# Kernel tuning notes

Measured on AMD Instinct MI355X. Metric: run time of the kernel, lower is better.

The kernel has to match this reference:

```python
import jax, jax.numpy as jnp
import numpy as np

B, T, E, D, V, L, A = 32, 800, 512, 1024, 5000, 149, 512
SOS, EOS = 1, 2


def setup_inputs() -> dict:
    key = jax.random.key(0)
    ks = jax.random.split(key, 20)
    s = 0.02
    inp = {
        'hpad': jax.random.normal(ks[0], (B, T, E), dtype=jnp.float32),
        'hlen': jax.random.randint(ks[1], (B,), T // 2, T + 1),
        'ys': jax.random.randint(ks[2], (B, L), 3, V),
        # embedding + output projection
        'embed': jax.random.normal(ks[3], (V, D), dtype=jnp.float32) * s,
        'W_out': jax.random.normal(ks[4], (V, D), dtype=jnp.float32) * s,
        'b_out': jnp.zeros((V,), dtype=jnp.float32),
        # additive attention params
        'W_enc': jax.random.normal(ks[5], (E, A), dtype=jnp.float32) * s,
        'W_dec': jax.random.normal(ks[6], (D, A), dtype=jnp.float32) * s,
        'v_att': jax.random.normal(ks[7], (A,), dtype=jnp.float32) * s,
        # LSTMCell layer 0: input = [ey; att_c] of size D+E
        'W_ih0': jax.random.normal(ks[8], (4 * D, D + E), dtype=jnp.float32) * s,
        'b_ih0': jnp.zeros((4 * D,), dtype=jnp.float32),
        'W_hh0': jax.random.normal(ks[9], (4 * D, D), dtype=jnp.float32) * s,
        'b_hh0': jnp.zeros((4 * D,), dtype=jnp.float32),
        # LSTMCell layer 1: input = z0 of size D
        'W_ih1': jax.random.normal(ks[10], (4 * D, D), dtype=jnp.float32) * s,
        'b_ih1': jnp.zeros((4 * D,), dtype=jnp.float32),
        'W_hh1': jax.random.normal(ks[11], (4 * D, D), dtype=jnp.float32) * s,
        'b_hh1': jnp.zeros((4 * D,), dtype=jnp.float32),
    }
    return inp


def _lstm_cell(x, h, c, W_ih, b_ih, W_hh, b_hh):
    # torch.nn.LSTMCell gate order: i, f, g, o
    g = x @ W_ih.T + b_ih + h @ W_hh.T + b_hh
    i, f, gg, o = jnp.split(g, 4, axis=-1)
    c2 = jax.nn.sigmoid(f) * c + jax.nn.sigmoid(i) * jnp.tanh(gg)
    h2 = jax.nn.sigmoid(o) * jnp.tanh(c2)
    return h2, c2


def reference(hpad, hlen, ys, embed, W_out, b_out, W_enc, W_dec, v_att,
              W_ih0, b_ih0, W_hh0, b_hh0, W_ih1, b_ih1, W_hh1, b_hh1):
    mask = jnp.arange(T)[None, :] < hlen[:, None]          # [B,T]
    hpad = hpad * mask[..., None]                          # mask_by_length
    ys_in = jnp.concatenate([jnp.full((B, 1), SOS, ys.dtype), ys], axis=1)   # [B,L+1]
    ys_out = jnp.concatenate([ys, jnp.full((B, 1), EOS, ys.dtype)], axis=1)  # [B,L+1]
    eys = embed[ys_in]                                     # [B,L+1,D]
    pe = jnp.einsum('bte,ea->bta', hpad, W_enc)            # precomputed enc proj

    def step(carry, ey):
        z0, c0, z1, c1 = carry
        # additive attention: e = v^T tanh(W_enc h + W_dec z0)
        e = jnp.einsum('bta,a->bt', jnp.tanh(pe + (z0 @ W_dec)[:, None, :]), v_att)
        e = jnp.where(mask, e, -1e30)
        w = jax.nn.softmax(e, axis=-1)                     # [B,T]
        att_c = jnp.einsum('bt,bte->be', w, hpad)          # [B,E]
        z0, c0 = _lstm_cell(jnp.concatenate([ey, att_c], axis=1), z0, c0,
                            W_ih0, b_ih0, W_hh0, b_hh0)
        z1, c1 = _lstm_cell(z0, z1, c1, W_ih1, b_ih1, W_hh1, b_hh1)
        logits = z1 @ W_out.T + b_out                      # [B,V]
        return (z0, c0, z1, c1), logits

    z = jnp.zeros((B, D), dtype=hpad.dtype)
    carry0 = (z, z, z, z)
    _, logits = jax.lax.scan(step, carry0, eys.transpose(1, 0, 2))  # [L+1,B,V]
    logits = logits.transpose(1, 0, 2)                     # [B,L+1,V]

    logp = jax.nn.log_softmax(logits, axis=-1)
    nll = -jnp.take_along_axis(logp, ys_out[..., None], axis=-1)[..., 0]
    # F.cross_entropy mean, then * (mean(len ys_in) - 1) = * L
    loss = nll.mean() * L
    acc = (jnp.argmax(logits, axis=-1) == ys_out).mean()
    return loss, acc
```

## Files before the change

kernel.cpp:

```cpp
#include <hip/hip_runtime.h>


typedef unsigned short u16;
typedef unsigned char u8;
typedef unsigned int u32;
typedef long long i64;
typedef unsigned long long u64;
typedef float f32x4 __attribute__((ext_vector_type(4)));
typedef float f32x2 __attribute__((ext_vector_type(2)));
typedef short s16x8 __attribute__((ext_vector_type(8)));

constexpr int cB = 32, cT = 800, cE = 512, cD = 1024, cV = 5000, cL = 149,
              cNS = 150, cA = 512;
constexpr int SOS = 1, EOS = 2;
constexpr int NBLK = 256;
constexpr float DS = 1.0f / 128.0f;

constexpr int AFLAG = 0;
constexpr int Z0FLAG = 256;
constexpr int Z1FLAG = 384;
constexpr int SFLAG = 512;
constexpr int ZDONE = 768;

__device__ __forceinline__ float bf2f(u16 x){
  union { u32 u; float f; } v; v.u = ((u32)x) << 16; return v.f;
}
__device__ __forceinline__ u16 f2bf(float f){
  union { float f; u32 u; } v; v.f = f;
  u32 r = v.u + 0x7FFFu + ((v.u >> 16) & 1u);
  return (u16)(r >> 16);
}
__device__ __forceinline__ float frcp(float x){ return __builtin_amdgcn_rcpf(x); }
__device__ __forceinline__ float fsigm(float x){ return frcp(1.f + __expf(-x)); }
__device__ __forceinline__ float ftanh(float x){
  float u = __expf(2.f * x);
  return 1.f - 2.f * frcp(u + 1.f);
}
__device__ __forceinline__ f32x4 MFMA(s16x8 a, s16x8 b, f32x4 c){
  return __builtin_amdgcn_mfma_f32_16x16x32_bf16(a, b, c, 0, 0, 0);
}
__device__ __forceinline__ f32x4 MFMA8(i64 a, i64 b, f32x4 c){
  return __builtin_amdgcn_mfma_f32_16x16x32_fp8_fp8(a, b, c, 0, 0, 0);
}
__device__ __forceinline__ s16x8 LD8(const u16* p){ return *(const s16x8*)p; }
__device__ __forceinline__ u8 f2fp8(float x){
// ... 36 lines not shown
}
__device__ __forceinline__ void atomic_pk_bf16(u32* dst, u32 data){
  asm volatile("global_atomic_pk_add_bf16 %0, %1, off"
               :: "v"(dst), "v"(data) : "memory");
}

__device__ __forceinline__ void pollge(const u32* f, int n, u32 target){
  const int lane = threadIdx.x & 63;
  for(;;){
    bool ok = true;
    for (int i = lane; i < n; i += 64) ok &= (ld_su(f + i) >= target);
    if (__all(ok)) break;
    __builtin_amdgcn_s_sleep(1);
  }
}
__device__ __forceinline__ void sig(u32* f, u32 v){
  asm volatile("s_waitcnt vmcnt(0)" ::: "memory");
  st_su(f, v);
}

__global__ void k_init(u32* ctl, u32* qt, float* c0, float* c1, u8* z1f8,
                       u32* att_pk, float* att_l, u32* hh1t){
  int i = blockIdx.x * blockDim.x + threadIdx.x, n = gridDim.x * blockDim.x;
  for (int k = i; k < 1024; k += n) ctl[k] = 0;
  for (int k = i; k < cB * cA; k += n) qt[k] = 0;
  for (int k = i; k < 2 * cB * cD; k += n){ c0[k] = 0.f; c1[k] = 0.f; }
  for (int k = i; k < cB * cD / 4; k += n) ((u32*)z1f8)[k] = 0;
  for (int k = i; k < 2 * cB * 256; k += n) att_pk[k] = 0;
  for (int k = i; k < 2 * cB; k += n) att_l[k] = 0.f;
  for (int k = i; k < cB * 4096; k += n) hh1t[k] = 0xFFFF0000u;
}

__global__ void k_cvt(const float* __restrict__ s, u16* __restrict__ d, int n4){
  int i = blockIdx.x * blockDim.x + threadIdx.x, st = gridDim.x * blockDim.x;
  for (int k = i; k < n4; k += st){
    float4 v = ((const float4*)s)[k];
    ushort4 o; o.x = f2bf(v.x); o.y = f2bf(v.y); o.z = f2bf(v.z); o.w = f2bf(v.w);
    ((ushort4*)d)[k] = o;
  }
}

__global__ void k_cvt8I(const float* __restrict__ s, u8* __restrict__ d, int n){
  int i = blockIdx.x * blockDim.x + threadIdx.x, st = gridDim.x * blockDim.x;
  for (int k = i; k < n; k += st){
    int row = k >> 6, grp = k & 63;
    const float4* p = (const float4*)(s + (size_t)row * 512 + grp * 8);
    float4 v0 = p[0], v1 = p[1];
// ... 9 lines not shown
  int cmask = (1 << cshift) - 1;
  for (int k = i; k < n; k += st){
    int r = k >> cshift, c = k & cmask;
    d[k] = f2bf(s[(size_t)r * srcld + coff + c]);
  }
}

__global__ void k_transp(const float* __restrict__ s, u16* __restrict__ d, int n,
                         int rshift, int csrc){
  int i = blockIdx.x * blockDim.x + threadIdx.x, st = gridDim.x * blockDim.x;
  int mask = (1 << rshift) - 1;
  for (int k = i; k < n; k += st){
    int dd = k & mask, a = k >> rshift;
    d[k] = f2bf(s[(size_t)dd * csrc + a]);
  }
}

__global__ void k_bias(const float* a, const float* b, float* o, int n){
  int i = blockIdx.x * blockDim.x + threadIdx.x, st = gridDim.x * blockDim.x;
  for (int k = i; k < n; k += st) o[k] = a[k] + b[k];
}

__global__ void k_wf8perm(const float* __restrict__ s, u8* __restrict__ d,
                          int n4, int kshift, int srcld, int coff){
  int i = blockIdx.x * blockDim.x + threadIdx.x, st = gridDim.x * blockDim.x;
  int kmask = (1 << kshift) - 1;
  for (int k = i; k < n4; k += st){
    int flat = k * 4;
    int R = flat >> kshift, kk = flat & kmask;
    int j = R >> 5, jj = R & 31, g = jj >> 3, c = jj & 7;
    const float* p = s + (size_t)(g * 1024 + j * 8 + c) * srcld + coff + kk;
    ((u32*)d)[k] = pk4(p[0]*16.f, p[1]*16.f, p[2]*16.f, p[3]*16.f);
  }
}

__global__ void k_wf8(const float* __restrict__ s, u8* __restrict__ d, int n4){
  int i = blockIdx.x * blockDim.x + threadIdx.x, st = gridDim.x * blockDim.x;
  for (int k = i; k < n4; k += st){
    float4 v = ((const float4*)s)[k];
    ((u32*)d)[k] = pk4(v.x*16.f, v.y*16.f, v.z*16.f, v.w*16.f);
  }
}

__global__ void k_wf8t(const float* __restrict__ s, u8* __restrict__ d, int n4){
  int i = blockIdx.x * blockDim.x + threadIdx.x, st = gridDim.x * blockDim.x;
  for (int k = i; k < n4; k += st){
    int flat = k * 4;
    int a = flat >> 10, dd = flat & 1023;
    ((u32*)d)[k] = pk4(s[(size_t)(dd+0)*512 + a]*16.f,
                       s[(size_t)(dd+1)*512 + a]*16.f,
                       s[(size_t)(dd+2)*512 + a]*16.f,
                       s[(size_t)(dd+3)*512 + a]*16.f);
  }
}
// ... 73 lines not shown
  int hi4 = (l >> 4) * 4;
  #pragma unroll
  for (int i = 0; i < 4; ++i)
    #pragma unroll
    for (int j = 0; j < 8; ++j){
      int jc = n0 + j * 16 + col;
      float bj = bih0[jc] + bhh0[jc];
      #pragma unroll
      for (int r = 0; r < 4; ++r){
        int row = m0 + i * 16 + hi4 + r;
        if (row < 4800){
          float val = acc[i][j][r] + bj;
          eyproj[(size_t)row * 4096 + jc] = f2bf(val);
          if (row < 32) g0t[(size_t)row * 4096 + jc] = (u32)f2bf(val);
        }
      }
    }
}

struct LoopArgs {
  const int* hlen;
  const u8* ph8;
  const u16* eyproj;
  const u8* Wapf8; const u8* Whh1f8; const u8* Wih1f8; const u8* Whh0f8;
  const u8* WdecTf8;
  const float* vatt; const float* bias01;
  u32* qt; u32* att_pk; float* att_l;
  u32* g0t; u32* hh1t; u8* z0f8; u8* z1f8;
  float* c0; float* c1; u16* z1all;
  u32* ctl;
};

constexpr int SPZ = 1048;
constexpr int SPA = 536;

struct P1Lds { float red[8][512]; float ls[8]; float qsh[512]; };
struct GvLds { u8 x[32 * SPZ]; float acc[8][2][16][17]; };
union LoopLds { P1Lds p1; GvLds gv; };

__device__ __forceinline__ void stage_att(LoopLds& L, const u32* att_pk,
                                          const float* att_l, int tid){
  int r = tid >> 4, cp = (tid & 15) * 16;
  float sc = 8.0f * frcp(ld_sc(att_l + r));
  const u32* src = att_pk + (size_t)r * 256 + cp;
  u64 v[8];
  #pragma unroll
  for (int i = 0; i < 8; ++i) v[i] = ld_sc8(src + i * 2);
// ... 25 lines not shown
template<int KH, int ITERS, int SP>
__device__ __forceinline__ void gemv_reg(const i64* wreg, LoopLds& L, int tid){
  const int w = tid >> 6, l = tid & 63;
  const int col = l & 15, kin = 8 * (l >> 4);
  const int kh = (KH == 4) ? (w & 3) : (w & 1);
  constexpr int KB = ITERS * 32;
  const u8* xr = &L.gv.x[col * SP + kh * KB + kin];
  f32x4 a0 = {0.f,0.f,0.f,0.f}, a1 = {0.f,0.f,0.f,0.f};
  #pragma unroll
  for (int kc = 0; kc < ITERS; ++kc){
    i64 x0 = *(const i64*)(xr + kc * 32);
    i64 x1 = *(const i64*)(xr + 16 * SP + kc * 32);
    a0 = MFMA8(x0, wreg[kc], a0);
    a1 = MFMA8(x1, wreg[kc], a1);
  }
  const int hi4 = (l >> 4) * 4;
  #pragma unroll
  for (int r = 0; r < 4; ++r){
    L.gv.acc[w][0][hi4 + r][col] = a0[r];
    L.gv.acc[w][1][hi4 + r][col] = a1[r];
  }
}

__global__ __launch_bounds__(512, 1) void k_loop(LoopArgs g_){
  __shared__ __align__(16) LoopLds L;
  __shared__ __align__(16) u8 ph8_lds[100 * 1024];
  const int blk = blockIdx.x, tid = threadIdx.x;
  const int w = tid >> 6, l = tid & 63;
  const int col = l & 15, kin = 8 * (l >> 4);
  const int b_att = blk >> 3, oct = blk & 7;
  const int hl = g_.hlen[b_att];
  const int t0 = oct * 100;
  const int t1 = (t0 + 100 < hl) ? t0 + 100 : hl;
  const int nrow = t1 - t0;
  u32* ctl = g_.ctl;
  float vv[8];
  #pragma unroll
  for (int i = 0; i < 8; ++i) vv[i] = g_.vatt[l * 8 + i];
  for (int idx = tid; idx < nrow * 64; idx += 512){
    int rr = idx >> 6, gg = idx & 63;
    *(uint4*)&ph8_lds[rr * 1024 + gg * 16] =
        *(const uint4*)(g_.ph8 + ((size_t)b_att * cT + t0 + rr) * 1024 + gg * 16);
  }
  i64 wB[8], wC[16];
  {
    const int nt4 = w >> 2, kh4 = w & 3;
    const int nt2 = w >> 1, kh2 = w & 1;
    if (blk < 128){
      const u8* wr = g_.Wapf8 + (size_t)blk * 32 * 512 +
                     (size_t)(nt4 * 16 + col) * 512 + kh4 * 128 + kin;
      #pragma unroll
      for (int kc = 0; kc < 4; ++kc) wB[kc] = *(const i64*)(wr + kc * 32);
      const u8* wr2 = g_.Wih1f8 + (size_t)blk * 32 * 1024 +
                      (size_t)(nt4 * 16 + col) * 1024 + kh4 * 256 + kin;
      #pragma unroll
      for (int kc = 0; kc < 8; ++kc) wC[kc] = *(const i64*)(wr2 + kc * 32);
    } else {
      const u8* wr = g_.Whh1f8 + (size_t)(blk - 128) * 32 * 1024 +
                     (size_t)(nt4 * 16 + col) * 1024 + kh4 * 256 + kin;
      #pragma unroll
      for (int kc = 0; kc < 8; ++kc) wB[kc] = *(const i64*)(wr + kc * 32);
      if (blk < 192){
        const u8* wr2 = g_.Whh0f8 + (size_t)(blk - 128) * 64 * 1024 +
                        (size_t)(nt2 * 16 + col) * 1024 + kh2 * 512 + kin;
        #pragma unroll
        for (int kc = 0; kc < 16; ++kc) wC[kc] = *(const i64*)(wr2 + kc * 32);
      } else if (blk < 208){
        const u8* wr2 = g_.WdecTf8 + (size_t)(blk - 192) * 32 * 1024 +
                        (size_t)(nt4 * 16 + col) * 1024 + kh4 * 256 + kin;
        #pragma unroll
        for (int kc = 0; kc < 8; ++kc) wC[kc] = *(const i64*)(wr2 + kc * 32);
      }
    }
  }
  __syncthreads();

  for (int s = 0; s < cNS; ++s){
    const int p = s & 1;
    if (nrow > 0){
      if (w == 0){
        const u32* qrow = g_.qt + b_att * cA + l * 8;
        const u64 tmask = 0xFFFF0000FFFF0000ULL;
        const u64 texp = ((u64)(u32)s << 48) | ((u64)(u32)s << 16);
        u64 qw[4];
        for(;;){
          bool ok = true;
          #pragma unroll
          for (int i = 0; i < 4; ++i){
            qw[i] = ld_sc8(qrow + i * 2);
            ok &= ((qw[i] & tmask) == texp);
          }
          if (l == 0)
            ok &= (ld_su(&ctl[ZDONE + p * 16]) >= (u32)(s >> 1));
          if (__all(ok)) break;
          __builtin_amdgcn_s_sleep(1);
        }
        #pragma unroll
        for (int i = 0; i < 4; ++i){
          L.p1.qsh[l * 8 + 2*i]     = bf2f((u16)(qw[i] & 0xFFFF));
          L.p1.qsh[l * 8 + 2*i + 1] = bf2f((u16)((qw[i] >> 32) & 0xFFFF));
        }
      }
      __syncthreads();
      float qv[8];
      #pragma unroll
      for (int i = 0; i < 8; ++i) qv[i] = L.p1.qsh[l * 8 + i];
      float acc8[8] = {0.f,0.f,0.f,0.f,0.f,0.f,0.f,0.f};
      float lsum = 0.f;
      for (int t = t0 + w; t < t1; t += 8){
        uint4 v = *(const uint4*)&ph8_lds[(t - t0) * 1024 + l * 16];
        float x[8]; unpack8(v.x, v.y, x);
        float e_ = 0.f;
        #pragma unroll
        for (int i = 0; i < 8; ++i) e_ += vv[i] * ftanh(x[i] + qv[i]);
        #pragma unroll
        for (int m = 1; m < 64; m <<= 1) e_ += __shfl_xor(e_, m, 64);
        float wt = __expf(e_);
        lsum += wt;
        float h[8]; unpack8(v.z, v.w, h);
        #pragma unroll
        for (int i = 0; i < 8; ++i) acc8[i] = fmaf(wt, h[i], acc8[i]);
      }
      *(f32x4*)&L.p1.red[w][l * 8]     = *(f32x4*)&acc8[0];
      *(f32x4*)&L.p1.red[w][l * 8 + 4] = *(f32x4*)&acc8[4];
      if (l == 0) L.p1.ls[w] = lsum;
      __syncthreads();
      if (tid < 256){
        float v0 = 0.f, v1 = 0.f;
        #pragma unroll
        for (int ww = 0; ww < 8; ++ww){
          v0 += L.p1.red[ww][tid * 2];
          v1 += L.p1.red[ww][tid * 2 + 1];
        }
        u32 pk = ((u32)f2bf(v1) << 16) | (u32)f2bf(v0);
        atomic_pk_bf16(g_.att_pk + ((size_t)p * cB + b_att) * 256 + tid, pk);
      }
      if (tid == 0){
        float ls = 0.f;
        #pragma unroll
        for (int i = 0; i < 8; ++i) ls += L.p1.ls[i];
        atomicAdd(&g_.att_l[p * cB + b_att], ls);
      }
    }
    __syncthreads();
    if (tid == 0) sig(&ctl[AFLAG + blk], (u32)(s + 1));
    if (blk < 128){
      if (tid < 64) pollge(ctl + AFLAG, 256, (u32)(s + 1));
      __syncthreads();
      stage_att(L, g_.att_pk + (size_t)p * cB * 256, g_.att_l + p * cB, tid);
      __syncthreads();
      if (tid == 0) sig(&ctl[SFLAG + p * 128 + blk], (u32)(s >> 1) + 1u);
      u32 gw[4]; bool gok = true; float cpre = 0.f;
      int bb = tid >> 3, dc = tid & 7, d = blk * 8 + dc;
      if (tid < 256){
        #pragma unroll
        for (int g = 0; g < 4; ++g){
          gw[g] = ld_su(&g_.g0t[(size_t)bb * 4096 + g * 1024 + d]);
          gok &= ((gw[g] >> 16) == (u32)s);
        }
        cpre = g_.c0[(size_t)p * cB * cD + bb * cD + d];
      }
      gemv_reg<4, 4, SPA>(wB, L, tid);
      __syncthreads();
      if (tid < 256){
        while (!__all(gok)){
          gok = true;
          #pragma unroll
          for (int g = 0; g < 4; ++g){
            gw[g] = ld_su(&g_.g0t[(size_t)bb * 4096 + g * 1024 + d]);
            gok &= ((gw[g] >> 16) == (u32)s);
          }
          if (!__all(gok)) __builtin_amdgcn_s_sleep(1);
        }
        int mt = bb >> 4, rr = bb & 15;
        float gate[4];
        #pragma unroll
        for (int g = 0; g < 4; ++g){
          int jj = g * 8 + dc;
          float v = 0.f;
          #pragma unroll
          for (int kh = 0; kh < 4; ++kh)
            v += L.gv.acc[(jj >> 4) * 4 + kh][mt][rr][jj & 15];
          gate[g] = v * DS + bf2f((u16)(gw[g] & 0xFFFF));
        }
        float c = fsigm(gate[1]) * cpre + fsigm(gate[0]) * ftanh(gate[2]);
        float z = fsigm(gate[3]) * ftanh(c);
        g_.c0[(size_t)(p ^ 1) * cB * cD + bb * cD + d] = c;
        st_scb(&g_.z0f8[bb * cD + d], f2fp8(z * 8.f));
      }
      __syncthreads();
      if (tid == 0) sig(&ctl[Z0FLAG + blk], (u32)(s + 1));
    } else {
      if (tid < 64) pollge(ctl + Z1FLAG, 128, (u32)s);
      __syncthreads();
      stage_z(L, g_.z1f8, tid);
      __syncthreads();
      gemv_reg<4, 8, SPZ>(wB, L, tid);
      __syncthreads();
      {
        const int jb = (blk - 128) * 32;
        int bb = tid >> 4, j2 = (tid & 15) * 2;
        int mt = bb >> 4, rr = bb & 15;
        u32 ow[2];
        #pragma unroll
        for (int k = 0; k < 2; ++k){
          int jj = j2 + k;
          float v = 0.f;
          #pragma unroll
          for (int kh = 0; kh < 4; ++kh)
            v += L.gv.acc[(jj >> 4) * 4 + kh][mt][rr][jj & 15];
          ow[k] = ((u32)(s + 1) << 16) | (u32)f2bf(v * DS + g_.bias01[jb + jj]);
        }
        st_sc8(&g_.hh1t[(size_t)bb * 4096 + jb + j2], ((u64)ow[1] << 32) | ow[0]);
      }
    }
    if (blk < 128){
      if (tid < 64) pollge(ctl + Z0FLAG, 128, (u32)(s + 1));
      __syncthreads();
      stage_z(L, g_.z0f8, tid);
      __syncthreads();
      u32 hw[4]; bool hok = true; float cpre = 0.f;
      int bb = tid >> 3, dc = tid & 7, d = blk * 8 + dc;
      if (tid < 256){
        #pragma unroll
        for (int g = 0; g < 4; ++g){
          hw[g] = ld_su(&g_.hh1t[(size_t)bb * 4096 + g * 1024 + d]);
          hok &= ((hw[g] >> 16) == (u32)(s + 1));
        }
        cpre = g_.c1[(size_t)p * cB * cD + bb * cD + d];
      }
      gemv_reg<4, 8, SPZ>(wC, L, tid);
      __syncthreads();
      if (tid < 256){
        while (!__all(hok)){
          hok = true;
          #pragma unroll
          for (int g = 0; g < 4; ++g){
            hw[g] = ld_su(&g_.hh1t[(size_t)bb * 4096 + g * 1024 + d]);
            hok &= ((hw[g] >> 16) == (u32)(s + 1));
          }
          if (!__all(hok)) __builtin_amdgcn_s_sleep(1);
        }
        int mt = bb >> 4, rr = bb & 15;
        float gate[4];
        #pragma unroll
        for (int g = 0; g < 4; ++g){
          int jj = g * 8 + dc;
          float v = 0.f;
          #pragma unroll
          for (int kh = 0; kh < 4; ++kh)
            v += L.gv.acc[(jj >> 4) * 4 + kh][mt][rr][jj & 15];
          gate[g] = v * DS + bf2f((u16)(hw[g] & 0xFFFF));
        }
        float c = fsigm(gate[1]) * cpre + fsigm(gate[0]) * ftanh(gate[2]);
        float z = fsigm(gate[3]) * ftanh(c);
        g_.c1[(size_t)(p ^ 1) * cB * cD + bb * cD + d] = c;
        g_.z1all[((size_t)s + 1) * cB * cD + bb * cD + d] = f2bf(z);
        st_scb(&g_.z1f8[bb * cD + d], f2fp8(z * 8.f));
      }
      __syncthreads();
      if (tid == 0) sig(&ctl[Z1FLAG + blk], (u32)(s + 1));
    } else if (blk < 192){
      if (tid < 64) pollge(ctl + Z0FLAG, 128, (u32)(s + 1));
      __syncthreads();
      stage_z(L, g_.z0f8, tid);
      __syncthreads();
      gemv_reg<2, 16, SPZ>(wC, L, tid);
      __syncthreads();
      if (s < cNS - 1){
        const int jb = (blk - 128) * 64;
        int bb = tid >> 4, j4 = (tid & 15) * 4;
        int mt = bb >> 4, rr = bb & 15;
        const u16* eyr = g_.eyproj + (((size_t)(s + 1) * cB + bb) * 4096) + jb + j4;
        u32 ow[4];
        #pragma unroll
        for (int k = 0; k < 4; ++k){
          int jj = j4 + k;
          float v = 0.f;
          #pragma unroll
          for (int kh = 0; kh < 2; ++kh)
            v += L.gv.acc[(jj >> 4) * 2 + kh][mt][rr][jj & 15];
          ow[k] = ((u32)(s + 1) << 16) | (u32)f2bf(v * DS + bf2f(eyr[k]));
        }
        st_sc8(&g_.g0t[(size_t)bb * 4096 + jb + j4],     ((u64)ow[1] << 32) | ow[0]);
        st_sc8(&g_.g0t[(size_t)bb * 4096 + jb + j4 + 2], ((u64)ow[3] << 32) | ow[2]);
      }
    } else if (blk < 208){
      if (tid < 64) pollge(ctl + Z0FLAG, 128, (u32)(s + 1));
      __syncthreads();
      stage_z(L, g_.z0f8, tid);
      __syncthreads();
      gemv_reg<4, 8, SPZ>(wC, L, tid);
      __syncthreads();
      if (s < cNS - 1){
        const int jb = (blk - 192) * 32;
        int bb = tid >> 4, j2 = (tid & 15) * 2;
        int mt = bb >> 4, rr = bb & 15;
        u32 ow[2];
        #pragma unroll
        for (int k = 0; k < 2; ++k){
          int jj = j2 + k;
          float v = 0.f;
          #pragma unroll
          for (int kh = 0; kh < 4; ++kh)
            v += L.gv.acc[(jj >> 4) * 4 + kh][mt][rr][jj & 15];
          ow[k] = ((u32)(s + 1) << 16) | (u32)f2bf(v * DS);
        }
        st_sc8(&g_.qt[(size_t)bb * cA + jb + j2], ((u64)ow[1] << 32) | ow[0]);
      }
    } else if (blk == 208){
      if (tid < 64) pollge(ctl + SFLAG + p * 128, 128, (u32)(s >> 1) + 1u);
      __syncthreads();
      {
        u32* aa = g_.att_pk + (size_t)p * cB * 256;
        for (int i = tid; i < cB * 256; i += 512) st_su(&aa[i], 0);
        if (tid < cB) st_sc(&g_.att_l[p * cB + tid], 0.f);
      }
      __syncthreads();
      if (tid == 0) sig(&ctl[ZDONE + p * 16], (u32)(s >> 1) + 1u);
    }
  }
}

__global__ __launch_bounds__(256) void k_ce1(const u16* __restrict__ z1all,
    const u16* __restrict__ Woutb, const float* __restrict__ bout,
    const int* __restrict__ ys, float* __restrict__ pmax, float* __restrict__ psum,
    int* __restrict__ pai, float* __restrict__ tgtl){
  int blk = blockIdx.x;
  int sc = blk / 40, vc = blk % 40;
  int tid = threadIdx.x, w = tid >> 6, l = tid & 63;
  int kin = 8 * (l >> 4), col = l & 15;
  int v0 = vc * 128 + w * 32;
  int vA = v0 + col, vB = v0 + 16 + col;
  float boA = (vA < cV) ? bout[vA] : 0.f;
// ... 118 lines not shown
  const int*   hlen = (const int*)d_in[1];
  const int*   ys   = (const int*)d_in[2];
  const float* embed= (const float*)d_in[3];
  const float* Wout = (const float*)d_in[4];
  const float* bout = (const float*)d_in[5];
  const float* Wenc = (const float*)d_in[6];
  const float* Wdec = (const float*)d_in[7];
  const float* vatt = (const float*)d_in[8];
  const float* Wih0 = (const float*)d_in[9];
  const float* bih0 = (const float*)d_in[10];
  const float* Whh0 = (const float*)d_in[11];
  const float* bhh0 = (const float*)d_in[12];
  const float* Wih1 = (const float*)d_in[13];
  const float* bih1 = (const float*)d_in[14];
  const float* Whh1 = (const float*)d_in[15];
  const float* bhh1 = (const float*)d_in[16];
  (void)in_sizes; (void)n_in; (void)out_size; (void)ws_size;

  char* base = (char*)d_ws;
  size_t off = 0;
  auto alloc = [&](size_t bytes) -> void* {
    void* r = base + off; off += (bytes + 255) & ~(size_t)255; return r;
  };
  u32*   ctl     = (u32*)  alloc(1024 * 4);
  u16*   hpadM   = (u16*)  alloc((size_t)cB * cT * cE * 2);
  u8*    ph8     = (u8*)   alloc((size_t)cB * cT * 1024);
  u16*   embb    = (u16*)  alloc((size_t)cV * cD * 2);
  u16*   ey      = (u16*)  alloc((size_t)cNS * cB * cD * 2);
  u16*   eyproj  = (u16*)  alloc((size_t)cNS * cB * 4096 * 2);
  u16*   z1all   = (u16*)  alloc((size_t)(cNS + 1) * cB * cD * 2);
  u16*   WencT   = (u16*)  alloc((size_t)cA * cE * 2);
  u16*   Wih0m   = (u16*)  alloc((size_t)4096 * cD * 2);
  u16*   Woutb   = (u16*)  alloc((size_t)cV * cD * 2);
  u8*    Wapf8   = (u8*)   alloc((size_t)4096 * 512);
  u8*    Wih1f8  = (u8*)   alloc((size_t)4096 * 1024);
  u8*    Whh1f8  = (u8*)   alloc((size_t)4096 * 1024);
  u8*    Whh0f8  = (u8*)   alloc((size_t)4096 * 1024);
  u8*    WdecTf8 = (u8*)   alloc((size_t)512 * 1024);
  float* bias01  = (float*)alloc(4096 * 4);
  u32*   qt      = (u32*)  alloc((size_t)cB * cA * 4);
  u32*   att_pk  = (u32*)  alloc((size_t)2 * cB * 256 * 4);
  float* att_l   = (float*)alloc((size_t)2 * cB * 4);
  u32*   g0t     = (u32*)  alloc((size_t)cB * 4096 * 4);
  u32*   hh1t    = (u32*)  alloc((size_t)cB * 4096 * 4);
  u8*    z0f8    = (u8*)   alloc((size_t)cB * cD);
  u8*    z1f8    = (u8*)   alloc((size_t)cB * cD);
  float* c0      = (float*)alloc((size_t)2 * cB * cD * 4);
  float* c1      = (float*)alloc((size_t)2 * cB * cD * 4);
  float* pmax    = (float*)alloc((size_t)cNS * cB * 40 * 4);
  float* psum    = (float*)alloc((size_t)cNS * cB * 40 * 4);
  int*   pai     = (int*)  alloc((size_t)cNS * cB * 40 * 4);
  float* tgtl    = (float*)alloc((size_t)cNS * cB * 4);
  float* cestep  = (float*)alloc((size_t)cNS * 2 * 4);

  k_init<<<64, 256, 0, stream>>>(ctl, qt, c0, c1, z1f8, att_pk, att_l, hh1t);
  k_cvt<<<2048, 256, 0, stream>>>(hpad, hpadM, cB * cT * cE / 4);
  k_cvt8I<<<1024, 256, 0, stream>>>(hpad, ph8, cB * cT * 64);
  k_cvt<<<2048, 256, 0, stream>>>(embed, embb, cV * cD / 4);
  k_cvt<<<2048, 256, 0, stream>>>(Wout, Woutb, cV * cD / 4);
  k_slice<<<1024, 256, 0, stream>>>(Wih0, Wih0m, 4096 * cD, 10, 1536, 0);
  k_transp<<<256, 256, 0, stream>>>(Wenc, WencT, cA * cE, 9, cA);
  k_bias<<<16, 256, 0, stream>>>(bih1, bhh1, bias01, 4096);
  k_wf8perm<<<512, 256, 0, stream>>>(Wih0, Wapf8, 4096 * 512 / 4, 9, 1536, 1024);
  k_wf8perm<<<1024, 256, 0, stream>>>(Wih1, Wih1f8, 4096 * 1024 / 4, 10, 1024, 0);
  k_wf8<<<1024, 256, 0, stream>>>(Whh1, Whh1f8, 4096 * 1024 / 4);
  k_wf8<<<1024, 256, 0, stream>>>(Whh0, Whh0f8, 4096 * 1024 / 4);
  k_wf8t<<<128, 256, 0, stream>>>(Wdec, WdecTf8, 512 * 1024 / 4);
  k_gather<<<1200, 256, 0, stream>>>(embb, ys, ey, cNS * cB * 128);
  k_pe2<<<200, 512, 0, stream>>>(hpadM, WencT, ph8);
  k_ey2<<<dim3(38, 8), 512, 0, stream>>>(ey, Wih0m, bih0, bhh0, eyproj, g0t);

  LoopArgs la;
  la.hlen = hlen; la.ph8 = ph8; la.eyproj = eyproj;
  la.Wapf8 = Wapf8; la.Whh1f8 = Whh1f8; la.Wih1f8 = Wih1f8;
  la.Whh0f8 = Whh0f8; la.WdecTf8 = WdecTf8;
  la.vatt = vatt; la.bias01 = bias01;
  la.qt = qt; la.att_pk = att_pk; la.att_l = att_l;
  la.g0t = g0t; la.hh1t = hh1t; la.z0f8 = z0f8; la.z1f8 = z1f8;
  la.c0 = c0; la.c1 = c1; la.z1all = z1all; la.ctl = ctl;
  k_loop<<<NBLK, 512, 0, stream>>>(la);

  k_ce1<<<1200, 256, 0, stream>>>(z1all, Woutb, bout, ys, pmax, psum, pai, tgtl);
  k_ce2<<<cNS, 64, 0, stream>>>(pmax, psum, pai, tgtl, ys, cestep);
  k_ce3<<<1, 256, 0, stream>>>(cestep, (float*)d_out);
}
```

Before: 4.028 ms.

## Split persistent loop into 512 blocks with dedicated attention blocks

Doubles the persistent decoder grid to 512 blocks. 256 blocks now do only the attention scoring and read the encoder projection straight from global memory instead of staging it in LDS. The other 256 blocks handle the LSTM layer-0 gate GEMV with 16 columns each, plus the Wdec, Wih1, Whh0 and Whh1 GEMVs, and z0 is double-buffered. The aim is to spread the per-step recurrent work over more CUs and free LDS so more blocks fit per CU. The cost is more flag polling across twice as many blocks, and attention now reads global/L2 memory every step.

```diff
diff --git a/kernel.cpp b/kernel.cpp
--- a/kernel.cpp
+++ b/kernel.cpp
@@ -13,14 +13,13 @@
 constexpr int cB = 32, cT = 800, cE = 512, cD = 1024, cV = 5000, cL = 149,
               cNS = 150, cA = 512;
 constexpr int SOS = 1, EOS = 2;
-constexpr int NBLK = 256;
 constexpr float DS = 1.0f / 128.0f;
 
 constexpr int AFLAG = 0;
 constexpr int Z0FLAG = 256;
-constexpr int Z1FLAG = 384;
-constexpr int SFLAG = 512;
-constexpr int ZDONE = 768;
+constexpr int Z1FLAG = 512;
+constexpr int SFLAG = 768;
+constexpr int ZDONE = 1536;
 
 __device__ __forceinline__ float bf2f(u16 x){
   union { u32 u; float f; } v; v.u = ((u32)x) << 16; return v.f;
@@ -103,7 +102,7 @@
 __global__ void k_init(u32* ctl, u32* qt, float* c0, float* c1, u8* z1f8,
                        u32* att_pk, float* att_l, u32* hh1t){
   int i = blockIdx.x * blockDim.x + threadIdx.x, n = gridDim.x * blockDim.x;
-  for (int k = i; k < 1024; k += n) ctl[k] = 0;
+  for (int k = i; k < 2048; k += n) ctl[k] = 0;
   for (int k = i; k < cB * cA; k += n) qt[k] = 0;
   for (int k = i; k < 2 * cB * cD; k += n){ c0[k] = 0.f; c1[k] = 0.f; }
   for (int k = i; k < cB * cD / 4; k += n) ((u32*)z1f8)[k] = 0;
@@ -159,14 +158,14 @@
 }
 
 __global__ void k_wf8perm(const float* __restrict__ s, u8* __restrict__ d,
-                          int n4, int kshift, int srcld, int coff){
+                          int n4, int kshift, int srcld, int coff, int gshift){
   int i = blockIdx.x * blockDim.x + threadIdx.x, st = gridDim.x * blockDim.x;
-  int kmask = (1 << kshift) - 1;
+  int kmask = (1 << kshift) - 1, gmask = (1 << gshift) - 1;
   for (int k = i; k < n4; k += st){
     int flat = k * 4;
     int R = flat >> kshift, kk = flat & kmask;
-    int j = R >> 5, jj = R & 31, g = jj >> 3, c = jj & 7;
-    const float* p = s + (size_t)(g * 1024 + j * 8 + c) * srcld + coff + kk;
+    int c = R & gmask, g = (R >> gshift) & 3, j = R >> (gshift + 2);
+    const float* p = s + (size_t)(g * 1024 + (j << gshift) + c) * srcld + coff + kk;
     ((u32*)d)[k] = pk4(p[0]*16.f, p[1]*16.f, p[2]*16.f, p[3]*16.f);
   }
 }
@@ -286,7 +285,7 @@
   const int* hlen;
   const u8* ph8;
   const u16* eyproj;
-  const u8* Wapf8; const u8* Whh1f8; const u8* Wih1f8; const u8* Whh0f8;
+  const u8* Wap16; const u8* Whh1f8; const u8* Wih1f8; const u8* Whh0f8;
   const u8* WdecTf8;
   const float* vatt; const float* bias01;
   u32* qt; u32* att_pk; float* att_l;
@@ -358,183 +357,160 @@
   }
 }
 
-__global__ __launch_bounds__(512, 1) void k_loop(LoopArgs g_){
+__device__ __forceinline__ void gemv16(const i64* wreg, LoopLds& L, int tid){
+  const int w = tid >> 6, l = tid & 63;
+  const int col = l & 15, kin = 8 * (l >> 4);
+  const u8* xr = &L.gv.x[col * SPA + w * 64 + kin];
+  f32x4 a0 = {0.f,0.f,0.f,0.f}, a1 = {0.f,0.f,0.f,0.f};
+  #pragma unroll
+  for (int kc = 0; kc < 2; ++kc){
+    i64 x0 = *(const i64*)(xr + kc * 32);
+    i64 x1 = *(const i64*)(xr + 16 * SPA + kc * 32);
+    a0 = MFMA8(x0, wreg[kc], a0);
+    a1 = MFMA8(x1, wreg[kc], a1);
+  }
+  const int hi4 = (l >> 4) * 4;
+  #pragma unroll
+  for (int r = 0; r < 4; ++r){
+    L.gv.acc[w][0][hi4 + r][col] = a0[r];
+    L.gv.acc[w][1][hi4 + r][col] = a1[r];
+  }
+}
+
+__global__ __launch_bounds__(512, 4) void k_loop(LoopArgs g_){
   __shared__ __align__(16) LoopLds L;
-  __shared__ __align__(16) u8 ph8_lds[100 * 1024];
   const int blk = blockIdx.x, tid = threadIdx.x;
   const int w = tid >> 6, l = tid & 63;
   const int col = l & 15, kin = 8 * (l >> 4);
-  const int b_att = blk >> 3, oct = blk & 7;
-  const int hl = g_.hlen[b_att];
-  const int t0 = oct * 100;
-  const int t1 = (t0 + 100 < hl) ? t0 + 100 : hl;
-  const int nrow = t1 - t0;
   u32* ctl = g_.ctl;
-  float vv[8];
-  #pragma unroll
-  for (int i = 0; i < 8; ++i) vv[i] = g_.vatt[l * 8 + i];
-  for (int idx = tid; idx < nrow * 64; idx += 512){
-    int rr = idx >> 6, gg = idx & 63;
-    *(uint4*)&ph8_lds[rr * 1024 + gg * 16] =
-        *(const uint4*)(g_.ph8 + ((size_t)b_att * cT + t0 + rr) * 1024 + gg * 16);
-  }
-  i64 wB[8], wC[16];
+
+  if (blk >= 256){
+    const int aid = blk - 256;
+    const int b_att = aid >> 3, oct = aid & 7;
+    const int hl = g_.hlen[b_att];
+    const int t0 = oct * 100;
+    const int t1 = (t0 + 100 < hl) ? t0 + 100 : hl;
+    const int nrow = t1 - t0;
+    float vv[8];
+    #pragma unroll
+    for (int i = 0; i < 8; ++i) vv[i] = g_.vatt[l * 8 + i];
+    const u8* phrow = g_.ph8 + ((size_t)b_att * cT) * 1024 + l * 16;
+    for (int s = 0; s < cNS; ++s){
+      const int p = s & 1;
+      if (nrow > 0){
+        if (w == 0){
+          const u32* qrow = g_.qt + b_att * cA + l * 8;
+          const u64 tmask = 0xFFFF0000FFFF0000ULL;
+          const u64 texp = ((u64)(u32)s << 48) | ((u64)(u32)s << 16);
+          u64 qw[4];
+          for(;;){
+            bool ok = true;
+            #pragma unroll
+            for (int i = 0; i < 4; ++i){
+              qw[i] = ld_sc8(qrow + i * 2);
+              ok &= ((qw[i] & tmask) == texp);
+            }
+            if (l == 0)
+              ok &= (ld_su(&ctl[ZDONE + p * 16]) >= (u32)(s >> 1));
+            if (__all(ok)) break;
+            __builtin_amdgcn_s_sleep(1);
+          }
+          #pragma unroll
+          for (int i = 0; i < 4; ++i){
+            L.p1.qsh[l * 8 + 2*i]     = bf2f((u16)(qw[i] & 0xFFFF));
+            L.p1.qsh[l * 8 + 2*i + 1] = bf2f((u16)((qw[i] >> 32) & 0xFFFF));
+          }
+        }
+        __syncthreads();
+        float qv[8];
+        #pragma unroll
+        for (int i = 0; i < 8; ++i) qv[i] = L.p1.qsh[l * 8 + i];
+        float acc8[8] = {0.f,0.f,0.f,0.f,0.f,0.f,0.f,0.f};
+        float lsum = 0.f;
+        for (int t = t0 + w; t < t1; t += 8){
+          uint4 v = *(const uint4*)(phrow + (size_t)t * 1024);
+          float x[8]; unpack8(v.x, v.y, x);
+          float e_ = 0.f;
+          #pragma unroll
+          for (int i = 0; i < 8; ++i) e_ += vv[i] * ftanh(x[i] + qv[i]);
+          #pragma unroll
+          for (int m = 1; m < 64; m <<= 1) e_ += __shfl_xor(e_, m, 64);
+          float wt = __expf(e_);
+          lsum += wt;
+          float h[8]; unpack8(v.z, v.w, h);
+          #pragma unroll
+          for (int i = 0; i < 8; ++i) acc8[i] = fmaf(wt, h[i], acc8[i]);
+        }
+        *(f32x4*)&L.p1.red[w][l * 8]     = *(f32x4*)&acc8[0];
+        *(f32x4*)&L.p1.red[w][l * 8 + 4] = *(f32x4*)&acc8[4];
+        if (l == 0) L.p1.ls[w] = lsum;
+        __syncthreads();
+        if (tid < 256){
+          float v0 = 0.f, v1 = 0.f;
+          #pragma unroll
+          for (int ww = 0; ww < 8; ++ww){
+            v0 += L.p1.red[ww][tid * 2];
+            v1 += L.p1.red[ww][tid * 2 + 1];
+          }
+          u32 pk = ((u32)f2bf(v1) << 16) | (u32)f2bf(v0);
+          atomic_pk_bf16(g_.att_pk + ((size_t)p * cB + b_att) * 256 + tid, pk);
+        }
+        if (tid == 0){
+          float ls = 0.f;
+          #pragma unroll
+          for (int i = 0; i < 8; ++i) ls += L.p1.ls[i];
+          atomicAdd(&g_.att_l[p * cB + b_att], ls);
+        }
+      }
+      __syncthreads();
+      if (tid == 0) sig(&ctl[AFLAG + aid], (u32)(s + 1));
+    }
+    return;
+  }
+
+  i64 wA[2], wH1[8], wX[16];
   {
     const int nt4 = w >> 2, kh4 = w & 3;
     const int nt2 = w >> 1, kh2 = w & 1;
+    const u8* wr = g_.Wap16 + (size_t)(blk * 16 + col) * 512 + w * 64 + kin;
+    #pragma unroll
+    for (int kc = 0; kc < 2; ++kc) wA[kc] = *(const i64*)(wr + kc * 32);
     if (blk < 128){
-      const u8* wr = g_.Wapf8 + (size_t)blk * 32 * 512 +
-                     (size_t)(nt4 * 16 + col) * 512 + kh4 * 128 + kin;
-      #pragma unroll
-      for (int kc = 0; kc < 4; ++kc) wB[kc] = *(const i64*)(wr + kc * 32);
-      const u8* wr2 = g_.Wih1f8 + (size_t)blk * 32 * 1024 +
-                      (size_t)(nt4 * 16 + col) * 1024 + kh4 * 256 + kin;
-      #pragma unroll
-      for (int kc = 0; kc < 8; ++kc) wC[kc] = *(const i64*)(wr2 + kc * 32);
-    } else {
-      const u8* wr = g_.Whh1f8 + (size_t)(blk - 128) * 32 * 1024 +
+      const u8* w1 = g_.Whh1f8 + (size_t)blk * 32 * 1024 +
                      (size_t)(nt4 * 16 + col) * 1024 + kh4 * 256 + kin;
       #pragma unroll
-      for (int kc = 0; kc < 8; ++kc) wB[kc] = *(const i64*)(wr + kc * 32);
-      if (blk < 192){
-        const u8* wr2 = g_.Whh0f8 + (size_t)(blk - 128) * 64 * 1024 +
-                        (size_t)(nt2 * 16 + col) * 1024 + kh2 * 512 + kin;
-        #pragma unroll
-        for (int kc = 0; kc < 16; ++kc) wC[kc] = *(const i64*)(wr2 + kc * 32);
-      } else if (blk < 208){
-        const u8* wr2 = g_.WdecTf8 + (size_t)(blk - 192) * 32 * 1024 +
-                        (size_t)(nt4 * 16 + col) * 1024 + kh4 * 256 + kin;
-        #pragma unroll
-        for (int kc = 0; kc < 8; ++kc) wC[kc] = *(const i64*)(wr2 + kc * 32);
-      }
+      for (int kc = 0; kc < 8; ++kc) wH1[kc] = *(const i64*)(w1 + kc * 32);
+    }
+    if (blk < 16){
+      const u8* w2 = g_.WdecTf8 + (size_t)blk * 32 * 1024 +
+                     (size_t)(nt4 * 16 + col) * 1024 + kh4 * 256 + kin;
+      #pragma unroll
+      for (int kc = 0; kc < 8; ++kc) wX[kc] = *(const i64*)(w2 + kc * 32);
+    } else if (blk < 144){
+      const u8* w2 = g_.Wih1f8 + (size_t)(blk - 16) * 32 * 1024 +
+                     (size_t)(nt4 * 16 + col) * 1024 + kh4 * 256 + kin;
+      #pragma unroll
+      for (int kc = 0; kc < 8; ++kc) wX[kc] = *(const i64*)(w2 + kc * 32);
+    } else if (blk < 208){
+      const u8* w2 = g_.Whh0f8 + (size_t)(blk - 144) * 64 * 1024 +
+                     (size_t)(nt2 * 16 + col) * 1024 + kh2 * 512 + kin;
+      #pragma unroll
+      for (int kc = 0; kc < 16; ++kc) wX[kc] = *(const i64*)(w2 + kc * 32);
     }
   }
   __syncthreads();
 
   for (int s = 0; s < cNS; ++s){
     const int p = s & 1;
-    if (nrow > 0){
-      if (w == 0){
-        const u32* qrow = g_.qt + b_att * cA + l * 8;
-        const u64 tmask = 0xFFFF0000FFFF0000ULL;
-        const u64 texp = ((u64)(u32)s << 48) | ((u64)(u32)s << 16);
-        u64 qw[4];
-        for(;;){
-          bool ok = true;
-          #pragma unroll
-          for (int i = 0; i < 4; ++i){
-            qw[i] = ld_sc8(qrow + i * 2);
-            ok &= ((qw[i] & tmask) == texp);
-          }
-          if (l == 0)
-            ok &= (ld_su(&ctl[ZDONE + p * 16]) >= (u32)(s >> 1));
-          if (__all(ok)) break;
-          __builtin_amdgcn_s_sleep(1);
-        }
-        #pragma unroll
-        for (int i = 0; i < 4; ++i){
-          L.p1.qsh[l * 8 + 2*i]     = bf2f((u16)(qw[i] & 0xFFFF));
-          L.p1.qsh[l * 8 + 2*i + 1] = bf2f((u16)((qw[i] >> 32) & 0xFFFF));
-        }
-      }
-      __syncthreads();
-      float qv[8];
-      #pragma unroll
-      for (int i = 0; i < 8; ++i) qv[i] = L.p1.qsh[l * 8 + i];
-      float acc8[8] = {0.f,0.f,0.f,0.f,0.f,0.f,0.f,0.f};
-      float lsum = 0.f;
-      for (int t = t0 + w; t < t1; t += 8){
-        uint4 v = *(const uint4*)&ph8_lds[(t - t0) * 1024 + l * 16];
-        float x[8]; unpack8(v.x, v.y, x);
-        float e_ = 0.f;
-        #pragma unroll
-        for (int i = 0; i < 8; ++i) e_ += vv[i] * ftanh(x[i] + qv[i]);
-        #pragma unroll
-        for (int m = 1; m < 64; m <<= 1) e_ += __shfl_xor(e_, m, 64);
-        float wt = __expf(e_);
-        lsum += wt;
-        float h[8]; unpack8(v.z, v.w, h);
-        #pragma unroll
-        for (int i = 0; i < 8; ++i) acc8[i] = fmaf(wt, h[i], acc8[i]);
-      }
-      *(f32x4*)&L.p1.red[w][l * 8]     = *(f32x4*)&acc8[0];
-      *(f32x4*)&L.p1.red[w][l * 8 + 4] = *(f32x4*)&acc8[4];
-      if (l == 0) L.p1.ls[w] = lsum;
-      __syncthreads();
-      if (tid < 256){
-        float v0 = 0.f, v1 = 0.f;
-        #pragma unroll
-        for (int ww = 0; ww < 8; ++ww){
-          v0 += L.p1.red[ww][tid * 2];
-          v1 += L.p1.red[ww][tid * 2 + 1];
-        }
-        u32 pk = ((u32)f2bf(v1) << 16) | (u32)f2bf(v0);
-        atomic_pk_bf16(g_.att_pk + ((size_t)p * cB + b_att) * 256 + tid, pk);
-      }
-      if (tid == 0){
-        float ls = 0.f;
-        #pragma unroll
-        for (int i = 0; i < 8; ++i) ls += L.p1.ls[i];
-        atomicAdd(&g_.att_l[p * cB + b_att], ls);
-      }
-    }
-    __syncthreads();
-    if (tid == 0) sig(&ctl[AFLAG + blk], (u32)(s + 1));
     if (blk < 128){
-      if (tid < 64) pollge(ctl + AFLAG, 256, (u32)(s + 1));
-      __syncthreads();
-      stage_att(L, g_.att_pk + (size_t)p * cB * 256, g_.att_l + p * cB, tid);
-      __syncthreads();
-      if (tid == 0) sig(&ctl[SFLAG + p * 128 + blk], (u32)(s >> 1) + 1u);
-      u32 gw[4]; bool gok = true; float cpre = 0.f;
-      int bb = tid >> 3, dc = tid & 7, d = blk * 8 + dc;
-      if (tid < 256){
-        #pragma unroll
-        for (int g = 0; g < 4; ++g){
-          gw[g] = ld_su(&g_.g0t[(size_t)bb * 4096 + g * 1024 + d]);
-          gok &= ((gw[g] >> 16) == (u32)s);
-        }
-        cpre = g_.c0[(size_t)p * cB * cD + bb * cD + d];
-      }
-      gemv_reg<4, 4, SPA>(wB, L, tid);
-      __syncthreads();
-      if (tid < 256){
-        while (!__all(gok)){
-          gok = true;
-          #pragma unroll
-          for (int g = 0; g < 4; ++g){
-            gw[g] = ld_su(&g_.g0t[(size_t)bb * 4096 + g * 1024 + d]);
-            gok &= ((gw[g] >> 16) == (u32)s);
-          }
-          if (!__all(gok)) __builtin_amdgcn_s_sleep(1);
-        }
-        int mt = bb >> 4, rr = bb & 15;
-        float gate[4];
-        #pragma unroll
-        for (int g = 0; g < 4; ++g){
-          int jj = g * 8 + dc;
-          float v = 0.f;
-          #pragma unroll
-          for (int kh = 0; kh < 4; ++kh)
-            v += L.gv.acc[(jj >> 4) * 4 + kh][mt][rr][jj & 15];
-          gate[g] = v * DS + bf2f((u16)(gw[g] & 0xFFFF));
-        }
-        float c = fsigm(gate[1]) * cpre + fsigm(gate[0]) * ftanh(gate[2]);
-        float z = fsigm(gate[3]) * ftanh(c);
-        g_.c0[(size_t)(p ^ 1) * cB * cD + bb * cD + d] = c;
-        st_scb(&g_.z0f8[bb * cD + d], f2fp8(z * 8.f));
-      }
-      __syncthreads();
-      if (tid == 0) sig(&ctl[Z0FLAG + blk], (u32)(s + 1));
-    } else {
       if (tid < 64) pollge(ctl + Z1FLAG, 128, (u32)s);
       __syncthreads();
       stage_z(L, g_.z1f8, tid);
       __syncthreads();
-      gemv_reg<4, 8, SPZ>(wB, L, tid);
+      gemv_reg<4, 8, SPZ>(wH1, L, tid);
       __syncthreads();
       {
-        const int jb = (blk - 128) * 32;
+        const int jb = blk * 32;
         int bb = tid >> 4, j2 = (tid & 15) * 2;
         int mt = bb >> 4, rr = bb & 15;
         u32 ow[2];
@@ -550,102 +526,140 @@
         st_sc8(&g_.hh1t[(size_t)bb * 4096 + jb + j2], ((u64)ow[1] << 32) | ow[0]);
       }
     }
-    if (blk < 128){
-      if (tid < 64) pollge(ctl + Z0FLAG, 128, (u32)(s + 1));
-      __syncthreads();
-      stage_z(L, g_.z0f8, tid);
-      __syncthreads();
-      u32 hw[4]; bool hok = true; float cpre = 0.f;
-      int bb = tid >> 3, dc = tid & 7, d = blk * 8 + dc;
-      if (tid < 256){
+    if (tid < 64) pollge(ctl + AFLAG, 256, (u32)(s + 1));
+    __syncthreads();
+    stage_att(L, g_.att_pk + (size_t)p * cB * 256, g_.att_l + p * cB, tid);
+    __syncthreads();
+    if (tid == 0) sig(&ctl[SFLAG + p * 256 + blk], (u32)(s >> 1) + 1u);
+    u32 gw[4]; bool gok = true; float cpre = 0.f;
+    int bb0 = tid >> 2, dc0 = tid & 3, d0 = blk * 4 + dc0;
+    if (tid < 128){
+      #pragma unroll
+      for (int g = 0; g < 4; ++g){
+        gw[g] = ld_su(&g_.g0t[(size_t)bb0 * 4096 + g * 1024 + d0]);
+        gok &= ((gw[g] >> 16) == (u32)s);
+      }
+      cpre = g_.c0[(size_t)p * cB * cD + bb0 * cD + d0];
+    }
+    gemv16(wA, L, tid);
+    __syncthreads();
+    if (tid < 128){
+      while (!__all(gok)){
+        gok = true;
         #pragma unroll
         for (int g = 0; g < 4; ++g){
-          hw[g] = ld_su(&g_.hh1t[(size_t)bb * 4096 + g * 1024 + d]);
-          hok &= ((hw[g] >> 16) == (u32)(s + 1));
-        }
-        cpre = g_.c1[(size_t)p * cB * cD + bb * cD + d];
-      }
-      gemv_reg<4, 8, SPZ>(wC, L, tid);
+          gw[g] = ld_su(&g_.g0t[(size_t)bb0 * 4096 + g * 1024 + d0]);
+          gok &= ((gw[g] >> 16) == (u32)s);
+        }
+        if (!__all(gok)) __builtin_amdgcn_s_sleep(1);
+      }
+      int mt = bb0 >> 4, rr = bb0 & 15;
+      float gate[4];
+      #pragma unroll
+      for (int g = 0; g < 4; ++g){
+        int jj = g * 4 + dc0;
+        float v = 0.f;
+        #pragma unroll
+        for (int w8 = 0; w8 < 8; ++w8) v += L.gv.acc[w8][mt][rr][jj];
+        gate[g] = v * DS + bf2f((u16)(gw[g] & 0xFFFF));
+      }
+      float c = fsigm(gate[1]) * cpre + fsigm(gate[0]) * ftanh(gate[2]);
+      float z = fsigm(gate[3]) * ftanh(c);
+      g_.c0[(size_t)(p ^ 1) * cB * cD + bb0 * cD + d0] = c;
+      st_scb(&g_.z0f8[(size_t)p * cB * cD + bb0 * cD + d0], f2fp8(z * 8.f));
+    }
+    __syncthreads();
+    if (tid == 0) sig(&ctl[Z0FLAG + blk], (u32)(s + 1));
+    if (blk < 208){
+      if (tid < 64) pollge(ctl + Z0FLAG, 256, (u32)(s + 1));
       __syncthreads();
-      if (tid < 256){
-        while (!__all(hok)){
-          hok = true;
+      stage_z(L, g_.z0f8 + (size_t)p * cB * cD, tid);
+      __syncthreads();
+      if (blk < 16){
+        gemv_reg<4, 8, SPZ>(wX, L, tid);
+        __syncthreads();
+        if (s < cNS - 1){
+          const int jb = blk * 32;
+          int bb = tid >> 4, j2 = (tid & 15) * 2;
+          int mt = bb >> 4, rr = bb & 15;
+          u32 ow[2];
+          #pragma unroll
+          for (int k = 0; k < 2; ++k){
+            int jj = j2 + k;
+            float v = 0.f;
+            #pragma unroll
+            for (int kh = 0; kh < 4; ++kh)
+              v += L.gv.acc[(jj >> 4) * 4 + kh][mt][rr][jj & 15];
+            ow[k] = ((u32)(s + 1) << 16) | (u32)f2bf(v * DS);
+          }
+          st_sc8(&g_.qt[(size_t)bb * cA + jb + j2], ((u64)ow[1] << 32) | ow[0]);
+        }
+      } else if (blk < 144){
+        u32 hw[4]; bool hok = true; float cpre1 = 0.f;
+        int bb = tid >> 3, dc = tid & 7, d = (blk - 16) * 8 + dc;
+        if (tid < 256){
           #pragma unroll
           for (int g = 0; g < 4; ++g){
             hw[g] = ld_su(&g_.hh1t[(size_t)bb * 4096 + g * 1024 + d]);
             hok &= ((hw[g] >> 16) == (u32)(s + 1));
           }
-          if (!__all(hok)) __builtin_amdgcn_s_sleep(1);
-        }
-        int mt = bb >> 4, rr = bb & 15;
-        float gate[4];
-        #pragma unroll
-        for (int g = 0; g < 4; ++g){
-          int jj = g * 8 + dc;
-          float v = 0.f;
-          #pragma unroll
-          for (int kh = 0; kh < 4; ++kh)
-            v += L.gv.acc[(jj >> 4) * 4 + kh][mt][rr][jj & 15];
-          gate[g] = v * DS + bf2f((u16)(hw[g] & 0xFFFF));
-        }
-        float c = fsigm(gate[1]) * cpre + fsigm(gate[0]) * ftanh(gate[2]);
-        float z = fsigm(gate[3]) * ftanh(c);
-        g_.c1[(size_t)(p ^ 1) * cB * cD + bb * cD + d] = c;
-        g_.z1all[((size_t)s + 1) * cB * cD + bb * cD + d] = f2bf(z);
-        st_scb(&g_.z1f8[bb * cD + d], f2fp8(z * 8.f));
-      }
-      __syncthreads();
-      if (tid == 0) sig(&ctl[Z1FLAG + blk], (u32)(s + 1));
-    } else if (blk < 192){
-      if (tid < 64) pollge(ctl + Z0FLAG, 128, (u32)(s + 1));
-      __syncthreads();
-      stage_z(L, g_.z0f8, tid);
-      __syncthreads();
-      gemv_reg<2, 16, SPZ>(wC, L, tid);
-      __syncthreads();
-      if (s < cNS - 1){
-        const int jb = (blk - 128) * 64;
-        int bb = tid >> 4, j4 = (tid & 15) * 4;
-        int mt = bb >> 4, rr = bb & 15;
-        const u16* eyr = g_.eyproj + (((size_t)(s + 1) * cB + bb) * 4096) + jb + j4;
-        u32 ow[4];
-        #pragma unroll
-        for (int k = 0; k < 4; ++k){
-          int jj = j4 + k;
-          float v = 0.f;
-          #pragma unroll
-          for (int kh = 0; kh < 2; ++kh)
-            v += L.gv.acc[(jj >> 4) * 2 + kh][mt][rr][jj & 15];
-          ow[k] = ((u32)(s + 1) << 16) | (u32)f2bf(v * DS + bf2f(eyr[k]));
-        }
-        st_sc8(&g_.g0t[(size_t)bb * 4096 + jb + j4],     ((u64)ow[1] << 32) | ow[0]);
-        st_sc8(&g_.g0t[(size_t)bb * 4096 + jb + j4 + 2], ((u64)ow[3] << 32) | ow[2]);
-      }
-    } else if (blk < 208){
-      if (tid < 64) pollge(ctl + Z0FLAG, 128, (u32)(s + 1));
-      __syncthreads();
-      stage_z(L, g_.z0f8, tid);
-      __syncthreads();
-      gemv_reg<4, 8, SPZ>(wC, L, tid);
-      __syncthreads();
-      if (s < cNS - 1){
-        const int jb = (blk - 192) * 32;
-        int bb = tid >> 4, j2 = (tid & 15) * 2;
-        int mt = bb >> 4, rr = bb & 15;
-        u32 ow[2];
-        #pragma unroll
-        for (int k = 0; k < 2; ++k){
-          int jj = j2 + k;
-          float v = 0.f;
-          #pragma unroll
-          for (int kh = 0; kh < 4; ++kh)
-            v += L.gv.acc[(jj >> 4) * 4 + kh][mt][rr][jj & 15];
-          ow[k] = ((u32)(s + 1) << 16) | (u32)f2bf(v * DS);
-        }
-        st_sc8(&g_.qt[(size_t)bb * cA + jb + j2], ((u64)ow[1] << 32) | ow[0]);
+          cpre1 = g_.c1[(size_t)p * cB * cD + bb * cD + d];
+        }
+        gemv_reg<4, 8, SPZ>(wX, L, tid);
+        __syncthreads();
+        if (tid < 256){
+          while (!__all(hok)){
+            hok = true;
+            #pragma unroll
+            for (int g = 0; g < 4; ++g){
+              hw[g] = ld_su(&g_.hh1t[(size_t)bb * 4096 + g * 1024 + d]);
+              hok &= ((hw[g] >> 16) == (u32)(s + 1));
+            }
+            if (!__all(hok)) __builtin_amdgcn_s_sleep(1);
+          }
+          int mt = bb >> 4, rr = bb & 15;
+          float gate[4];
+          #pragma unroll
+          for (int g = 0; g < 4; ++g){
+            int jj = g * 8 + dc;
+            float v = 0.f;
+            #pragma unroll
+            for (int kh = 0; kh < 4; ++kh)
+              v += L.gv.acc[(jj >> 4) * 4 + kh][mt][rr][jj & 15];
+            gate[g] = v * DS + bf2f((u16)(hw[g] & 0xFFFF));
+          }
+          float c = fsigm(gate[1]) * cpre1 + fsigm(gate[0]) * ftanh(gate[2]);
+          float z = fsigm(gate[3]) * ftanh(c);
+          g_.c1[(size_t)(p ^ 1) * cB * cD + bb * cD + d] = c;
+          g_.z1all[((size_t)s + 1) * cB * cD + bb * cD + d] = f2bf(z);
+          st_scb(&g_.z1f8[bb * cD + d], f2fp8(z * 8.f));
+        }
+        __syncthreads();
+        if (tid == 0) sig(&ctl[Z1FLAG + (blk - 16)], (u32)(s + 1));
+      } else {
+        gemv_reg<2, 16, SPZ>(wX, L, tid);
+        __syncthreads();
+        if (s < cNS - 1){
+          const int jb = (blk - 144) * 64;
+          int bb = tid >> 4, j4 = (tid & 15) * 4;
+          int mt = bb >> 4, rr = bb & 15;
+          const u16* eyr = g_.eyproj + (((size_t)(s + 1) * cB + bb) * 4096) + jb + j4;
+          u32 ow[4];
+          #pragma unroll
+          for (int k = 0; k < 4; ++k){
+            int jj = j4 + k;
+            float v = 0.f;
+            #pragma unroll
+            for (int kh = 0; kh < 2; ++kh)
+              v += L.gv.acc[(jj >> 4) * 2 + kh][mt][rr][jj & 15];
+            ow[k] = ((u32)(s + 1) << 16) | (u32)f2bf(v * DS + bf2f(eyr[k]));
+          }
+          st_sc8(&g_.g0t[(size_t)bb * 4096 + jb + j4],     ((u64)ow[1] << 32) | ow[0]);
+          st_sc8(&g_.g0t[(size_t)bb * 4096 + jb + j4 + 2], ((u64)ow[3] << 32) | ow[2]);
+        }
       }
     } else if (blk == 208){
-      if (tid < 64) pollge(ctl + SFLAG + p * 128, 128, (u32)(s >> 1) + 1u);
+      if (tid < 64) pollge(ctl + SFLAG + p * 256, 256, (u32)(s >> 1) + 1u);
       __syncthreads();
       {
         u32* aa = g_.att_pk + (size_t)p * cB * 256;
@@ -810,7 +824,7 @@
   auto alloc = [&](size_t bytes) -> void* {
     void* r = base + off; off += (bytes + 255) & ~(size_t)255; return r;
   };
-  u32*   ctl     = (u32*)  alloc(1024 * 4);
+  u32*   ctl     = (u32*)  alloc(2048 * 4);
   u16*   hpadM   = (u16*)  alloc((size_t)cB * cT * cE * 2);
   u8*    ph8     = (u8*)   alloc((size_t)cB * cT * 1024);
   u16*   embb    = (u16*)  alloc((size_t)cV * cD * 2);
@@ -820,7 +834,7 @@
   u16*   WencT   = (u16*)  alloc((size_t)cA * cE * 2);
   u16*   Wih0m   = (u16*)  alloc((size_t)4096 * cD * 2);
   u16*   Woutb   = (u16*)  alloc((size_t)cV * cD * 2);
-  u8*    Wapf8   = (u8*)   alloc((size_t)4096 * 512);
+  u8*    Wap16   = (u8*)   alloc((size_t)4096 * 512);
   u8*    Wih1f8  = (u8*)   alloc((size_t)4096 * 1024);
   u8*    Whh1f8  = (u8*)   alloc((size_t)4096 * 1024);
   u8*    Whh0f8  = (u8*)   alloc((size_t)4096 * 1024);
@@ -831,7 +845,7 @@
   float* att_l   = (float*)alloc((size_t)2 * cB * 4);
   u32*   g0t     = (u32*)  alloc((size_t)cB * 4096 * 4);
   u32*   hh1t    = (u32*)  alloc((size_t)cB * 4096 * 4);
-  u8*    z0f8    = (u8*)   alloc((size_t)cB * cD);
+  u8*    z0f8    = (u8*)   alloc((size_t)2 * cB * cD);
   u8*    z1f8    = (u8*)   alloc((size_t)cB * cD);
   float* c0      = (float*)alloc((size_t)2 * cB * cD * 4);
   float* c1      = (float*)alloc((size_t)2 * cB * cD * 4);
@@ -849,8 +863,8 @@
   k_slice<<<1024, 256, 0, stream>>>(Wih0, Wih0m, 4096 * cD, 10, 1536, 0);
   k_transp<<<256, 256, 0, stream>>>(Wenc, WencT, cA * cE, 9, cA);
   k_bias<<<16, 256, 0, stream>>>(bih1, bhh1, bias01, 4096);
-  k_wf8perm<<<512, 256, 0, stream>>>(Wih0, Wapf8, 4096 * 512 / 4, 9, 1536, 1024);
-  k_wf8perm<<<1024, 256, 0, stream>>>(Wih1, Wih1f8, 4096 * 1024 / 4, 10, 1024, 0);
+  k_wf8perm<<<512, 256, 0, stream>>>(Wih0, Wap16, 4096 * 512 / 4, 9, 1536, 1024, 2);
+  k_wf8perm<<<1024, 256, 0, stream>>>(Wih1, Wih1f8, 4096 * 1024 / 4, 10, 1024, 0, 3);
   k_wf8<<<1024, 256, 0, stream>>>(Whh1, Whh1f8, 4096 * 1024 / 4);
   k_wf8<<<1024, 256, 0, stream>>>(Whh0, Whh0f8, 4096 * 1024 / 4);
   k_wf8t<<<128, 256, 0, stream>>>(Wdec, WdecTf8, 512 * 1024 / 4);
@@ -860,13 +874,13 @@
 
   LoopArgs la;
   la.hlen = hlen; la.ph8 = ph8; la.eyproj = eyproj;
-  la.Wapf8 = Wapf8; la.Whh1f8 = Whh1f8; la.Wih1f8 = Wih1f8;
+  la.Wap16 = Wap16; la.Whh1f8 = Whh1f8; la.Wih1f8 = Wih1f8;
   la.Whh0f8 = Whh0f8; la.WdecTf8 = WdecTf8;
   la.vatt = vatt; la.bias01 = bias01;
   la.qt = qt; la.att_pk = att_pk; la.att_l = att_l;
   la.g0t = g0t; la.hh1t = hh1t; la.z0f8 = z0f8; la.z1f8 = z1f8;
   la.c0 = c0; la.c1 = c1; la.z1all = z1all; la.ctl = ctl;
-  k_loop<<<NBLK, 512, 0, stream>>>(la);
+  k_loop<<<512, 512, 0, stream>>>(la);
 
   k_ce1<<<1200, 256, 0, stream>>>(z1all, Woutb, bout, ys, pmax, psum, pai, tgtl);
   k_ce2<<<cNS, 64, 0, stream>>>(pmax, psum, pai, tgtl, ys, cestep);
```

New measurement: 5.511 ms. +36.8%, slower.
